# Optimization experiments

Measured on AMD Instinct MI355X. Metric: run time of the kernel, lower is better.

## Reference

```python
import jax, jax.numpy as jnp
import numpy as np

B, S, D, H, DH = 2, 4096, 768, 12, 64

def setup_inputs() -> dict:
    key = jax.random.key(0)
    kx, kq, kk, kv = jax.random.split(key, 4)
    x = jax.random.normal(kx, (B, S, D), dtype=jnp.float32)
    # per-head Q/K/V projection weights, stacked over heads: [H, d_in, d_out]
    Wq = jax.random.normal(kq, (H, D, DH), dtype=jnp.float32) * 0.02
    Wk = jax.random.normal(kk, (H, D, DH), dtype=jnp.float32) * 0.02
    Wv = jax.random.normal(kv, (H, D, DH), dtype=jnp.float32) * 0.02
    return {"x": x, "Wq": Wq, "Wk": Wk, "Wv": Wv}

def reference(x, Wq, Wk, Wv):
    b, s, _ = x.shape
    # per-head linear projections (qkv_bias=False), batched over heads
    q = jnp.einsum('bsd,hde->bhse', x, Wq)  # [B,H,S,DH]
    k = jnp.einsum('bsd,hde->bhse', x, Wk)
    v = jnp.einsum('bsd,hde->bhse', x, Wv)
    scale = 1.0 / jnp.sqrt(jnp.asarray(q.shape[-1], q.dtype))
    scores = jnp.einsum('bhqe,bhke->bhqk', q, k) * scale  # [B,H,S,S]
    causal_mask = jnp.triu(jnp.ones((s, s), dtype=bool), k=1)
    scores = jnp.where(causal_mask, -jnp.inf, scores)
    attn = jax.nn.softmax(scores, axis=-1)  # dropout p=0 -> identity
    ctx = jnp.einsum('bhqk,bhke->bhqe', attn, v)  # [B,H,S,DH]
    # concat heads on last dim (matches torch.cat of per-head outputs)
    return ctx.transpose(0, 2, 1, 3).reshape(b, s, -1)  # [B,S,H*DH]
```

## Files before the change

### kernel.cpp

```cpp
#include <hip/hip_runtime.h>
#include <hip/hip_bf16.h>
#include <stdint.h>

#define B_  2
#define S_  4096
#define D_  768
#define H_  12
#define DH_ 64
#define BS_ (B_*S_)

typedef __bf16 bf16x8 __attribute__((ext_vector_type(8)));
typedef short  svec8  __attribute__((ext_vector_type(8)));
typedef float  fvec4  __attribute__((ext_vector_type(4)));
typedef int    ivec4  __attribute__((ext_vector_type(4)));
typedef unsigned short ushort_t;

__device__ __forceinline__ ushort_t f2bf(float f){
    unsigned u = __builtin_bit_cast(unsigned, f);
    unsigned r = (u + 0x7fffu + ((u >> 16) & 1u)) >> 16;
    return (ushort_t)r;
}

__device__ __forceinline__ unsigned cvt_pk_bf16(float lo, float hi){
    unsigned r;
    asm("v_cvt_pk_bf16_f32 %0, %1, %2" : "=v"(r) : "v"(lo), "v"(hi));
    return r;
}

__device__ __forceinline__ fvec4 mfma16(svec8 a, svec8 b, fvec4 c){
    return __builtin_amdgcn_mfma_f32_16x16x32_bf16(
        __builtin_bit_cast(bf16x8, a), __builtin_bit_cast(bf16x8, b), c, 0, 0, 0);
}

__global__ __launch_bounds__(256, 3) void qkv_proj(
    const float* __restrict__ X,
    const float* __restrict__ Wq, const float* __restrict__ Wk, const float* __restrict__ Wv,
    ushort_t* __restrict__ Qb, ushort_t* __restrict__ Kb, ushort_t* __restrict__ Vg)
{
    const int m0 = blockIdx.x * 128;
    const int h  = blockIdx.y;
    const float* Whs[3] = { Wq + (size_t)h * (D_ * DH_),
                            Wk + (size_t)h * (D_ * DH_),
                            Wv + (size_t)h * (D_ * DH_) };

    __shared__ ushort_t smem[128 * 72 + 3 * 64 * 64];
    ushort_t* Xs  = smem;
    ushort_t* Wts = smem + 128 * 72;
    ushort_t* XsT = smem;

    const int tid  = threadIdx.x;
    const int w    = tid >> 6;
    const int lane = tid & 63;
    const int quad = lane >> 4;
    const int l15  = lane & 15;

    fvec4 acc[3][2][4];
    #pragma unroll
    for (int wt = 0; wt < 3; wt++)
        #pragma unroll
        for (int i = 0; i < 2; i++)
            #pragma unroll
            for (int j = 0; j < 4; j++) acc[wt][i][j] = (fvec4){0.f, 0.f, 0.f, 0.f};

    for (int k0 = 0; k0 < D_; k0 += 64) {
        #pragma unroll
        for (int i = 0; i < 4; i++) {
            int v = tid + 256 * i;
            int r = v >> 3, c = (v & 7) * 8;
            const float* src = X + (size_t)(m0 + r) * D_ + k0 + c;
            float4 d0 = *(const float4*)(src);
            float4 d1 = *(const float4*)(src + 4);
            svec8 pk;
            pk[0] = (short)f2bf(d0.x); pk[1] = (short)f2bf(d0.y);
            pk[2] = (short)f2bf(d0.z); pk[3] = (short)f2bf(d0.w);
            pk[4] = (short)f2bf(d1.x); pk[5] = (short)f2bf(d1.y);
            pk[6] = (short)f2bf(d1.z); pk[7] = (short)f2bf(d1.w);
            *(svec8*)(Xs + r * 72 + c) = pk;
        }
        #pragma unroll
        for (int wt = 0; wt < 3; wt++)
            #pragma unroll
            for (int i = 0; i < 4; i++) {
                int v = tid + 256 * i;
                int k = v >> 4, t = v & 15;
                float4 d = *(const float4*)(Whs[wt] + (size_t)(k0 + k) * DH_ + t * 4);
                #pragma unroll
                for (int j = 0; j < 4; j++) {
                    int n = t * 4 + j;
                    int addr = wt * 4096 + n * 64 + ((((k >> 3) ^ (t & 7))) << 3) + (k & 7);
                    Wts[addr] = f2bf(j == 0 ? d.x : j == 1 ? d.y : j == 2 ? d.z : d.w);
                }
            }
        __syncthreads();

        #pragma unroll
        for (int ks = 0; ks < 2; ks++) {
            svec8 a0 = *(const svec8*)(Xs + (32 * w + l15) * 72 + ks * 32 + quad * 8);
            svec8 a1 = *(const svec8*)(Xs + (32 * w + 16 + l15) * 72 + ks * 32 + quad * 8);
            #pragma unroll
            for (int wt = 0; wt < 3; wt++)
                #pragma unroll
                for (int ns = 0; ns < 4; ns++) {
                    int n = ns * 16 + l15;
                    int swz = (ks * 4 + quad) ^ ((n >> 2) & 7);
                    svec8 b = *(const svec8*)(Wts + wt * 4096 + n * 64 + swz * 8);
                    acc[wt][0][ns] = mfma16(a0, b, acc[wt][0][ns]);
                    acc[wt][1][ns] = mfma16(a1, b, acc[wt][1][ns]);
                }
        }
        __syncthreads();
    }

    const float qs = 0.18033688011112042f;
    #pragma unroll
    for (int ms = 0; ms < 2; ms++)
        #pragma unroll
        for (int ns = 0; ns < 4; ns++)
            #pragma unroll
            for (int r = 0; r < 4; r++) {
                int row = m0 + 32 * w + ms * 16 + quad * 4 + r;
                int col = h * DH_ + ns * 16 + l15;
                Qb[(size_t)row * D_ + col] = f2bf(acc[0][ms][ns][r] * qs);
                Kb[(size_t)row * D_ + col] = f2bf(acc[1][ms][ns][r]);
            }
    #pragma unroll
    for (int ms = 0; ms < 2; ms++)
        #pragma unroll
        for (int ns = 0; ns < 4; ns++)
            #pragma unroll
            for (int r = 0; r < 4; r++) {
                int sl = 32 * w + ms * 16 + quad * 4 + r;
                int e  = ns * 16 + l15;
                XsT[e * 136 + sl] = f2bf(acc[2][ms][ns][r]);
            }
    __syncthreads();
    #pragma unroll
    for (int i = 0; i < 4; i++) {
        int v = tid + 256 * i;
        int e = v >> 4, s0 = (v & 15) * 8;
        svec8 d = *(const svec8*)(XsT + e * 136 + s0);
        *(svec8*)(Vg + (size_t)(h * DH_ + e) * BS_ + m0 + s0) = d;
    }
}

__global__ __launch_bounds__(256, 5) void attn(
    const ushort_t* __restrict__ Qb, const ushort_t* __restrict__ Kb,
    const ushort_t* __restrict__ Vg, float* __restrict__ Out)
{
    const int fid = blockIdx.x;
    const int qt  = (S_ / 64 - 1) - fid / (H_ * B_);
    const int r24 = fid % (H_ * B_);
    const int h   = r24 % H_;
    const int b   = r24 / H_;
    const int q0 = qt * 64;

    const int tid  = threadIdx.x;
    const int w    = tid >> 6;
    const int lane = tid & 63;
    const int quad = lane >> 4;
    const int l15  = lane & 15;

    __shared__ ushort_t Ks[64 * 72];
    __shared__ ushort_t Vt[64 * 72];

    const size_t hb = (size_t)b * S_ * D_ + (size_t)h * DH_;
    const ushort_t* Vh = Vg + (size_t)h * DH_ * BS_ + (size_t)b * S_;

    const int sr = tid >> 3;
    const int sc = (tid & 7) * 8;
    const int pr0 = (((sr      >> 2) & 1) << 5) | (((sr      >> 5) & 1) << 4) |
                    (((sr      >> 4) & 1) << 3) | (((sr      >> 3) & 1) << 2) | (sr & 3);
    const int sr1 = sr + 32;
    const int pr1 = (((sr1 >> 2) & 1) << 5) | (((sr1 >> 5) & 1) << 4) |
                    (((sr1 >> 4) & 1) << 3) | (((sr1 >> 3) & 1) << 2) | (sr1 & 3);

    svec8 aq[2];
    {
        const ushort_t* qrow = Qb + hb + (size_t)(q0 + 16 * w + l15) * D_;
        aq[0] = *(const svec8*)(qrow + quad * 8);
        aq[1] = *(const svec8*)(qrow + 32 + quad * 8);
    }

    float m_i = -INFINITY;
    float ls  = 0.f;
    fvec4 acc[4];
    #pragma unroll
    for (int n = 0; n < 4; n++) acc[n] = (fvec4){0.f, 0.f, 0.f, 0.f};

    const ushort_t* kp = Kb + hb + (size_t)sr * D_ + sc;
    const ushort_t* vp = Vh + (size_t)sr * BS_ + sc;

    svec8 kd[2], vd[2];
    kd[0] = *(const svec8*)(kp);
    kd[1] = *(const svec8*)(kp + (size_t)32 * D_);
    vd[0] = *(const svec8*)(vp);
    vd[1] = *(const svec8*)(vp + (size_t)32 * BS_);
    kp += (size_t)64 * D_;
    vp += 64;
    *(svec8*)(Ks + pr0 * 72 + sc) = kd[0];
    *(svec8*)(Ks + pr1 * 72 + sc) = kd[1];
    *(svec8*)(Vt + sr  * 72 + sc) = vd[0];
    *(svec8*)(Vt + sr1 * 72 + sc) = vd[1];

    for (int kt = 0; kt <= qt; ++kt) {
        __syncthreads();

        if (kt < qt) {
            kd[0] = *(const svec8*)(kp);
            kd[1] = *(const svec8*)(kp + (size_t)32 * D_);
            vd[0] = *(const svec8*)(vp);
            vd[1] = *(const svec8*)(vp + (size_t)32 * BS_);
            kp += (size_t)64 * D_;
            vp += 64;
        }

        fvec4 st[4];
        #pragma unroll
        for (int n = 0; n < 4; n++) st[n] = (fvec4){0.f, 0.f, 0.f, 0.f};
        #pragma unroll
        for (int ks = 0; ks < 2; ks++)
            #pragma unroll
            for (int n = 0; n < 4; n++) {
                svec8 ka = *(const svec8*)(Ks + (n * 16 + l15) * 72 + ks * 32 + quad * 8);
                st[n] = mfma16(ka, aq[ks], st[n]);
            }

        if (kt == qt) {
            #pragma unroll
            for (int n = 0; n < 4; n++)
                #pragma unroll
                for (int r = 0; r < 4; r++) {
                    int key = (n & 1) * 32 + quad * 8 + (n >> 1) * 4 + r;
                    int row = 16 * w + l15;
                    if (key > row) st[n][r] = -INFINITY;
                }
        }

        float mxa = fmaxf(fmaxf(st[0][0], st[0][1]), st[0][2]);
        mxa = fmaxf(fmaxf(mxa, st[0][3]), st[1][0]);
        mxa = fmaxf(fmaxf(mxa, st[1][1]), st[1][2]);
        mxa = fmaxf(mxa, st[1][3]);
        float mxb = fmaxf(fmaxf(st[2][0], st[2][1]), st[2][2]);
        mxb = fmaxf(fmaxf(mxb, st[2][3]), st[3][0]);
        mxb = fmaxf(fmaxf(mxb, st[3][1]), st[3][2]);
        mxb = fmaxf(mxb, st[3][3]);
        float mx = fmaxf(mxa, mxb);
        mx = fmaxf(mx, __shfl_xor(mx, 16));
        mx = fmaxf(mx, __shfl_xor(mx, 32));

        if (__any(mx > m_i)) {
            float mn = fmaxf(m_i, mx);
            float alpha = exp2f(m_i - mn);
            m_i = mn;
            ls *= alpha;
            float ar[4];
            #pragma unroll
            for (int r = 0; r < 4; r++)
                ar[r] = __shfl(alpha, quad * 16 + quad * 4 + r);
            #pragma unroll
            for (int n = 0; n < 4; n++)
                #pragma unroll
                for (int r = 0; r < 4; r++) acc[n][r] *= ar[r];
        }

        ivec4 ai0, ai1;
        float psum[4];
        #pragma unroll
        for (int n = 0; n < 4; n++) {
            float p0 = exp2f(st[n][0] - m_i);
            float p1 = exp2f(st[n][1] - m_i);
            float p2 = exp2f(st[n][2] - m_i);
            float p3 = exp2f(st[n][3] - m_i);
            psum[n] = (p0 + p1) + (p2 + p3);
            unsigned d0 = cvt_pk_bf16(p0, p1);
            unsigned d1 = cvt_pk_bf16(p2, p3);
            if (n == 0)      { ai0[0] = (int)d0; ai0[1] = (int)d1; }
            else if (n == 1) { ai1[0] = (int)d0; ai1[1] = (int)d1; }
            else if (n == 2) { ai0[2] = (int)d0; ai0[3] = (int)d1; }
            else             { ai1[2] = (int)d0; ai1[3] = (int)d1; }
        }
        ls += (psum[0] + psum[2]) + (psum[1] + psum[3]);
        svec8 ap0 = __builtin_bit_cast(svec8, ai0);
        svec8 ap1 = __builtin_bit_cast(svec8, ai1);

        #pragma unroll
        for (int ks = 0; ks < 2; ks++) {
            svec8 ap = ks ? ap1 : ap0;
            #pragma unroll
            for (int n = 0; n < 4; n++) {
                svec8 bv = *(const svec8*)(Vt + (n * 16 + l15) * 72 + ks * 32 + quad * 8);
                acc[n] = mfma16(ap, bv, acc[n]);
            }
        }

        __syncthreads();

        if (kt < qt) {
            *(svec8*)(Ks + pr0 * 72 + sc) = kd[0];
            *(svec8*)(Ks + pr1 * 72 + sc) = kd[1];
            *(svec8*)(Vt + sr  * 72 + sc) = vd[0];
            *(svec8*)(Vt + sr1 * 72 + sc) = vd[1];
        }
    }

    float lsum = ls;
    lsum += __shfl_xor(lsum, 16);
    lsum += __shfl_xor(lsum, 32);
    float li[4];
    #pragma unroll
    for (int r = 0; r < 4; r++)
        li[r] = __shfl(lsum, quad * 16 + quad * 4 + r);
    #pragma unroll
    for (int n = 0; n < 4; n++)
        #pragma unroll
        for (int r = 0; r < 4; r++) {
            int row = q0 + 16 * w + quad * 4 + r;
            int col = h * DH_ + n * 16 + l15;
            Out[((size_t)b * S_ + row) * D_ + col] = acc[n][r] / li[r];
        }
}

extern "C" void kernel_launch(void* const* d_in, const int* in_sizes, int n_in,
                              void* d_out, int out_size, void* d_ws, size_t ws_size,
                              hipStream_t stream)
{
    const float* X  = (const float*)d_in[0];
    const float* Wq = (const float*)d_in[1];
    const float* Wk = (const float*)d_in[2];
    const float* Wv = (const float*)d_in[3];

    ushort_t* Qb = (ushort_t*)d_ws;
    ushort_t* Kb = Qb + (size_t)BS_ * D_;
    ushort_t* Vg = Kb + (size_t)BS_ * D_;
    float* Out = (float*)d_out;

    qkv_proj<<<dim3(64, H_), dim3(256), 0, stream>>>(X, Wq, Wk, Wv, Qb, Kb, Vg);
    attn<<<dim3((S_ / 64) * H_ * B_), dim3(256), 0, stream>>>(Qb, Kb, Vg, Out);
}
```

Measured before the change: 262.8 us.

## Pre-convert X and weights to bf16 in a separate prep kernel

```diff
diff --git a/kernel.cpp b/kernel.cpp
--- a/kernel.cpp
+++ b/kernel.cpp
@@ -15,10 +15,8 @@
 typedef int    ivec4  __attribute__((ext_vector_type(4)));
 typedef unsigned short ushort_t;
 
-__device__ __forceinline__ ushort_t f2bf(float f){
-    unsigned u = __builtin_bit_cast(unsigned, f);
-    unsigned r = (u + 0x7fffu + ((u >> 16) & 1u)) >> 16;
-    return (ushort_t)r;
+__device__ __forceinline__ ushort_t bfc(float f){
+    return __builtin_bit_cast(ushort_t, (__bf16)f);
 }
 
 __device__ __forceinline__ unsigned cvt_pk_bf16(float lo, float hi){
@@ -32,18 +30,49 @@
         __builtin_bit_cast(bf16x8, a), __builtin_bit_cast(bf16x8, b), c, 0, 0, 0);
 }
 
-__global__ __launch_bounds__(256, 3) void qkv_proj(
+__global__ __launch_bounds__(256) void prep(
     const float* __restrict__ X,
     const float* __restrict__ Wq, const float* __restrict__ Wk, const float* __restrict__ Wv,
+    ushort_t* __restrict__ Xb, ushort_t* __restrict__ Wsz)
+{
+    const int bid = blockIdx.x;
+    if (bid < 3072) {
+        size_t idx = ((size_t)bid * 256 + threadIdx.x) * 8;
+        float4 d0 = *(const float4*)(X + idx);
+        float4 d1 = *(const float4*)(X + idx + 4);
+        bf16x8 pk;
+        pk[0] = (__bf16)d0.x; pk[1] = (__bf16)d0.y;
+        pk[2] = (__bf16)d0.z; pk[3] = (__bf16)d0.w;
+        pk[4] = (__bf16)d1.x; pk[5] = (__bf16)d1.y;
+        pk[6] = (__bf16)d1.z; pk[7] = (__bf16)d1.w;
+        *(svec8*)(Xb + idx) = __builtin_bit_cast(svec8, pk);
+    } else {
+        const int v  = bid - 3072;
+        const int wt = v % 3;
+        const int hk = v / 3;
+        const int h  = hk / 12, kt = hk % 12;
+        const float* W  = (wt == 0) ? Wq : (wt == 1) ? Wk : Wv;
+        const float* Wh = W + (size_t)h * (D_ * DH_) + (size_t)kt * 64 * DH_;
+        ushort_t* dst = Wsz + (size_t)(hk * 3 + wt) * 4096;
+        #pragma unroll
+        for (int i = 0; i < 16; i++) {
+            int idx = threadIdx.x * 16 + i;
+            int k = idx >> 6, n = idx & 63;
+            float val = Wh[k * DH_ + n];
+            int addr = n * 64 + ((((k >> 3) ^ ((n >> 2) & 7))) << 3) + (k & 7);
+            dst[addr] = bfc(val);
+        }
+    }
+}
+
+__global__ __launch_bounds__(256, 3) void qkv_proj(
+    const ushort_t* __restrict__ Xb, const ushort_t* __restrict__ Wsz,
     ushort_t* __restrict__ Qb, ushort_t* __restrict__ Kb, ushort_t* __restrict__ Vg)
 {
     const int m0 = blockIdx.x * 128;
     const int h  = blockIdx.y;
-    const float* Whs[3] = { Wq + (size_t)h * (D_ * DH_),
-                            Wk + (size_t)h * (D_ * DH_),
-                            Wv + (size_t)h * (D_ * DH_) };
-
-    __shared__ ushort_t smem[128 * 72 + 3 * 64 * 64];
+
+    __shared__ ushort_t smem[128 * 72 + 3 * 4096];
     ushort_t* Xs  = smem;
     ushort_t* Wts = smem + 128 * 72;
     ushort_t* XsT = smem;
@@ -62,35 +91,21 @@
             #pragma unroll
             for (int j = 0; j < 4; j++) acc[wt][i][j] = (fvec4){0.f, 0.f, 0.f, 0.f};
 
-    for (int k0 = 0; k0 < D_; k0 += 64) {
+    for (int kt = 0; kt < 12; kt++) {
+        const int k0 = kt * 64;
         #pragma unroll
         for (int i = 0; i < 4; i++) {
             int v = tid + 256 * i;
             int r = v >> 3, c = (v & 7) * 8;
-            const float* src = X + (size_t)(m0 + r) * D_ + k0 + c;
-            float4 d0 = *(const float4*)(src);
-            float4 d1 = *(const float4*)(src + 4);
-            svec8 pk;
-            pk[0] = (short)f2bf(d0.x); pk[1] = (short)f2bf(d0.y);
-            pk[2] = (short)f2bf(d0.z); pk[3] = (short)f2bf(d0.w);
-            pk[4] = (short)f2bf(d1.x); pk[5] = (short)f2bf(d1.y);
-            pk[6] = (short)f2bf(d1.z); pk[7] = (short)f2bf(d1.w);
-            *(svec8*)(Xs + r * 72 + c) = pk;
-        }
-        #pragma unroll
-        for (int wt = 0; wt < 3; wt++)
-            #pragma unroll
-            for (int i = 0; i < 4; i++) {
-                int v = tid + 256 * i;
-                int k = v >> 4, t = v & 15;
-                float4 d = *(const float4*)(Whs[wt] + (size_t)(k0 + k) * DH_ + t * 4);
-                #pragma unroll
-                for (int j = 0; j < 4; j++) {
-                    int n = t * 4 + j;
-                    int addr = wt * 4096 + n * 64 + ((((k >> 3) ^ (t & 7))) << 3) + (k & 7);
-                    Wts[addr] = f2bf(j == 0 ? d.x : j == 1 ? d.y : j == 2 ? d.z : d.w);
-                }
-            }
+            *(svec8*)(Xs + r * 72 + c) =
+                *(const svec8*)(Xb + (size_t)(m0 + r) * D_ + k0 + c);
+        }
+        const ushort_t* wsrc = Wsz + (size_t)(h * 12 + kt) * 3 * 4096;
+        #pragma unroll
+        for (int j = 0; j < 6; j++) {
+            int lin = (tid + 256 * j) * 8;
+            *(svec8*)(Wts + lin) = *(const svec8*)(wsrc + lin);
+        }
         __syncthreads();
 
         #pragma unroll
@@ -120,8 +135,8 @@
             for (int r = 0; r < 4; r++) {
                 int row = m0 + 32 * w + ms * 16 + quad * 4 + r;
                 int col = h * DH_ + ns * 16 + l15;
-                Qb[(size_t)row * D_ + col] = f2bf(acc[0][ms][ns][r] * qs);
-                Kb[(size_t)row * D_ + col] = f2bf(acc[1][ms][ns][r]);
+                Qb[(size_t)row * D_ + col] = bfc(acc[0][ms][ns][r] * qs);
+                Kb[(size_t)row * D_ + col] = bfc(acc[1][ms][ns][r]);
             }
     #pragma unroll
     for (int ms = 0; ms < 2; ms++)
@@ -131,7 +146,7 @@
             for (int r = 0; r < 4; r++) {
                 int sl = 32 * w + ms * 16 + quad * 4 + r;
                 int e  = ns * 16 + l15;
-                XsT[e * 136 + sl] = f2bf(acc[2][ms][ns][r]);
+                XsT[e * 136 + sl] = bfc(acc[2][ms][ns][r]);
             }
     __syncthreads();
     #pragma unroll
@@ -332,8 +347,12 @@
     ushort_t* Qb = (ushort_t*)d_ws;
     ushort_t* Kb = Qb + (size_t)BS_ * D_;
     ushort_t* Vg = Kb + (size_t)BS_ * D_;
+
+    ushort_t* Xb  = (ushort_t*)d_out;
+    ushort_t* Wsz = Xb + (size_t)BS_ * D_;
     float* Out = (float*)d_out;
 
-    qkv_proj<<<dim3(64, H_), dim3(256), 0, stream>>>(X, Wq, Wk, Wv, Qb, Kb, Vg);
+    prep<<<dim3(3072 + 432), dim3(256), 0, stream>>>(X, Wq, Wk, Wv, Xb, Wsz);
+    qkv_proj<<<dim3(64, H_), dim3(256), 0, stream>>>(Xb, Wsz, Qb, Kb, Vg);
     attn<<<dim3((S_ / 64) * H_ * B_), dim3(256), 0, stream>>>(Qb, Kb, Vg, Out);
 }
```

Result: faster. 246.7 us (-6.1%).
